# Optimization experiments

Measured on AMD Instinct MI355X. Metric: run time of the kernel, lower is better.

The kernel has to match this reference:

```python
import jax, jax.numpy as jnp
import numpy as np

N, E, H, L, G = 50000, 800000, 128, 4, 64

def setup_inputs() -> dict:
    key = jax.random.key(0)
    ks = jax.random.split(key, 16)
    s = 0.05
    x = jax.random.normal(ks[0], (N, H), jnp.float32)
    edge_index = jax.random.randint(ks[1], (2, E), 0, N)
    edge_attr = jax.random.normal(ks[2], (E, 1), jnp.float32)
    # sorted graph assignment covering all G graphs (batch[-1]+1 == G)
    batch = (jnp.arange(N) * G) // N
    conv_W1 = jax.random.normal(ks[3], (L, H, H), jnp.float32) * s
    conv_b1 = jnp.zeros((L, H), jnp.float32)
    conv_W2 = jax.random.normal(ks[4], (L, H, H), jnp.float32) * s
    conv_b2 = jnp.zeros((L, H), jnp.float32)
    conv_eps = jnp.zeros((L,), jnp.float32)  # torch init: eps = 0
    edge_W = jax.random.normal(ks[5], (L, 1, H), jnp.float32) * s
    edge_b = jnp.zeros((L, H), jnp.float32)
    vn_W1 = jax.random.normal(ks[6], (L - 1, H, H), jnp.float32) * s
    vn_b1 = jnp.zeros((L - 1, H), jnp.float32)
    vn_W2 = jax.random.normal(ks[7], (L - 1, H, H), jnp.float32) * s
    vn_b2 = jnp.zeros((L - 1, H), jnp.float32)
    vn_emb = jnp.zeros((H,), jnp.float32)  # torch init: constant 0
    return dict(x=x, edge_attr=edge_attr, conv_W1=conv_W1, conv_b1=conv_b1,
                conv_W2=conv_W2, conv_b2=conv_b2, conv_eps=conv_eps,
                edge_W=edge_W, edge_b=edge_b, vn_W1=vn_W1, vn_b1=vn_b1,
                vn_W2=vn_W2, vn_b2=vn_b2, vn_emb=vn_emb,
                edge_index=edge_index, batch=batch)


def reference(x, edge_attr, conv_W1, conv_b1, conv_W2, conv_b2, conv_eps,
              edge_W, edge_b, vn_W1, vn_b1, vn_W2, vn_b2, vn_emb,
              edge_index, batch):
    src, tgt = edge_index[0], edge_index[1]
    # PyG mean aggregation: divide scatter-sum by in-degree (clamped to 1)
    deg = jnp.maximum(
        jax.ops.segment_sum(jnp.ones((E,), x.dtype), tgt, num_segments=N), 1.0)[:, None]
    vn = jnp.broadcast_to(vn_emb[None, :], (G, H))  # virtual node per graph
    h = x
    hs = []
    for i in range(L):
        h = h + vn[batch]
        edge_emb = edge_attr @ edge_W[i] + edge_b[i]          # [E,H]
        msg = jax.nn.relu(h[src] + edge_emb)                   # gather + relu
        agg = jax.ops.segment_sum(msg, tgt, num_segments=N) / deg  # mean scatter
        z = (1.0 + conv_eps[i]) * h + agg
        h = jax.nn.relu(z @ conv_W1[i] + conv_b1[i]) @ conv_W2[i] + conv_b2[i]
        hs.append(h)
        if i < L - 1:
            vt = jax.ops.segment_sum(hs[i], batch, num_segments=G) + vn
            vn = jax.nn.relu(
                jax.nn.relu(vt @ vn_W1[i] + vn_b1[i]) @ vn_W2[i] + vn_b2[i])
            # eval mode: dropout is identity
    return jnp.concatenate(hs, axis=1)  # [N, L*H] jumping-knowledge concat
```

## Files before the change

kernel.cpp:

```cpp
#include <hip/hip_runtime.h>

#define NN 50000
#define EE 800000
#define HH 128
#define LL 4
#define GG 64
#define NR 50048
#define NS 8
#define CAP 64

typedef short bf16x8 __attribute__((ext_vector_type(8)));
typedef float f32x4 __attribute__((ext_vector_type(4)));

__device__ __forceinline__ unsigned bf_round(float f) {
  unsigned u = __float_as_uint(f);
  return (u + 0x7fffu + ((u >> 16) & 1u)) >> 16;
}
__device__ __forceinline__ unsigned bf_pack2(float lo, float hi) {
  return bf_round(lo) | (bf_round(hi) << 16);
}

__global__ __launch_bounds__(256) void init_pack0_kernel(
    int initB,
    const float* __restrict__ W1, const float* __restrict__ W2,
    const float* __restrict__ emb, short* __restrict__ wt1, short* __restrict__ wt2,
    float* __restrict__ vnA, float* __restrict__ part01, int* __restrict__ cur,
    const float4* __restrict__ x4, const float* __restrict__ eb0,
    uint2* __restrict__ hbf, int N) {
  int bid = blockIdx.x;
  int t = threadIdx.x;
  const int NW = 2 * LL * HH * HH;
  const int R1 = NW + GG * HH;
  const int R2 = R1 + 2 * GG * HH;
  const int R3 = R2 + NN;
  if (bid < initB) {
    int idx = bid * 256 + t;
    if (idx < NW) {
      int m = idx >> 14;
      int r = idx & 16383;
      int n = r >> 7, k = r & 127;
      const float* W = (m < LL) ? (W1 + (size_t)m * 16384) : (W2 + (size_t)(m - LL) * 16384);
      short* D = (m < LL) ? (wt1 + (size_t)m * 16384) : (wt2 + (size_t)(m - LL) * 16384);
      D[n * 128 + k] = (short)bf_round(W[k * 128 + n]);
    } else if (idx < R1) {
      int i = idx - NW;
      vnA[i] = emb[i & (HH - 1)];
    } else if (idx < R2) {
      part01[idx - R1] = 0.f;
    } else if (idx < R3) {
      cur[idx - R2] = 0;
    }
    return;
  }
  int pidx = (bid - initB) * 256 + t;
  if (pidx >= N * (HH / 4)) return;
  int c4 = pidx & 31;
  float4 a = x4[pidx];
  const float4 v = *(const float4*)(emb + c4 * 4);
  const float4 e = *(const float4*)(eb0 + c4 * 4);
  uint2 o;
  o.x = bf_pack2(a.x + v.x + e.x, a.y + v.y + e.y);
  o.y = bf_pack2(a.z + v.z + e.z, a.w + v.w + e.w);
  hbf[pidx] = o;
}

__global__ __launch_bounds__(256) void scatter_kernel(const int* __restrict__ src,
                                                      const int* __restrict__ tgt,
                                                      const float* __restrict__ attr,
                                                      int* __restrict__ cur,
                                                      int2* __restrict__ es, int E) {
  int e = blockIdx.x * 256 + threadIdx.x;
  if (e < E) {
    int t = tgt[e];
    int p = atomicAdd(&cur[t], 1);
    int2 rec;
    rec.x = src[e];
    rec.y = __float_as_int(attr[e]);
    es[(size_t)t * CAP + p] = rec;
  }
}

__device__ __forceinline__ void accum8s(float* acc, uint4 p, float a, float m,
                                        const float4& ew0, const float4& ew1) {
  acc[0] = fmaf(m, fmaxf(fmaf(a, ew0.x, __uint_as_float(p.x << 16)), 0.f), acc[0]);
  acc[1] = fmaf(m, fmaxf(fmaf(a, ew0.y, __uint_as_float(p.x & 0xffff0000u)), 0.f), acc[1]);
  acc[2] = fmaf(m, fmaxf(fmaf(a, ew0.z, __uint_as_float(p.y << 16)), 0.f), acc[2]);
  acc[3] = fmaf(m, fmaxf(fmaf(a, ew0.w, __uint_as_float(p.y & 0xffff0000u)), 0.f), acc[3]);
  acc[4] = fmaf(m, fmaxf(fmaf(a, ew1.x, __uint_as_float(p.z << 16)), 0.f), acc[4]);
  acc[5] = fmaf(m, fmaxf(fmaf(a, ew1.y, __uint_as_float(p.z & 0xffff0000u)), 0.f), acc[5]);
  acc[6] = fmaf(m, fmaxf(fmaf(a, ew1.z, __uint_as_float(p.w << 16)), 0.f), acc[6]);
  acc[7] = fmaf(m, fmaxf(fmaf(a, ew1.w, __uint_as_float(p.w & 0xffff0000u)), 0.f), acc[7]);
}

__global__ __launch_bounds__(128) void agg_kernel(const uint4* __restrict__ hbf4,
                                                  const float* __restrict__ hp, int pitch,
                                                  const float* __restrict__ vnp,
                                                  const int* __restrict__ batch,
                                                  const int2* __restrict__ es,
                                                  const int* __restrict__ cnp,
                                                  const float* __restrict__ eW,
                                                  const float* __restrict__ epsp,
                                                  uint4* __restrict__ zb4, int N) {
  int wave = threadIdx.x >> 6;
  int lane = threadIdx.x & 63;
  int n = blockIdx.x * 2 + wave;
  if (n >= N) return;
  int q = lane >> 4;
  int c = lane & 15;
  float4 ew0 = *(const float4*)(eW + c * 8);
  float4 ew1 = *(const float4*)(eW + c * 8 + 4);
  int cnt = cnp[n];
  const int2* eb = es + (size_t)n * CAP;
  float acc[8];
#pragma unroll
  for (int j = 0; j < 8; ++j) acc[j] = 0.f;
  for (int k = 0; k < cnt; k += 16) {
    int2 e0 = eb[min(k + q, cnt - 1)];
    int2 e1 = eb[min(k + 4 + q, cnt - 1)];
    int2 e2 = eb[min(k + 8 + q, cnt - 1)];
    int2 e3 = eb[min(k + 12 + q, cnt - 1)];
    uint4 p0 = hbf4[(size_t)e0.x * 16 + c];
    uint4 p1 = hbf4[(size_t)e1.x * 16 + c];
    uint4 p2 = hbf4[(size_t)e2.x * 16 + c];
    uint4 p3 = hbf4[(size_t)e3.x * 16 + c];
    float m0 = (k + q < cnt) ? 1.f : 0.f;
    float m1 = (k + 4 + q < cnt) ? 1.f : 0.f;
    float m2 = (k + 8 + q < cnt) ? 1.f : 0.f;
    float m3 = (k + 12 + q < cnt) ? 1.f : 0.f;
    accum8s(acc, p0, __int_as_float(e0.y), m0, ew0, ew1);
    accum8s(acc, p1, __int_as_float(e1.y), m1, ew0, ew1);
    accum8s(acc, p2, __int_as_float(e2.y), m2, ew0, ew1);
    accum8s(acc, p3, __int_as_float(e3.y), m3, ew0, ew1);
  }
#pragma unroll
  for (int j = 0; j < 8; ++j) {
    acc[j] += __shfl_xor(acc[j], 16);
    acc[j] += __shfl_xor(acc[j], 32);
  }
  int g = batch[n];
  const float* hrow = hp + (size_t)n * pitch + c * 8;
  const float* vrow = vnp + g * HH + c * 8;
  float4 h0 = *(const float4*)(hrow);
  float4 h1 = *(const float4*)(hrow + 4);
  float4 v0 = *(const float4*)(vrow);
  float4 v1 = *(const float4*)(vrow + 4);
  float inv = 1.f / fmaxf((float)cnt, 1.f);
  float onep = 1.f + epsp[0];
  uint4 o;
  o.x = bf_pack2(fmaf(onep, h0.x + v0.x, acc[0] * inv),
                 fmaf(onep, h0.y + v0.y, acc[1] * inv));
  o.y = bf_pack2(fmaf(onep, h0.z + v0.z, acc[2] * inv),
                 fmaf(onep, h0.w + v0.w, acc[3] * inv));
  o.z = bf_pack2(fmaf(onep, h1.x + v1.x, acc[4] * inv),
                 fmaf(onep, h1.y + v1.y, acc[5] * inv));
  o.w = bf_pack2(fmaf(onep, h1.z + v1.z, acc[6] * inv),
                 fmaf(onep, h1.w + v1.w, acc[7] * inv));
  if (q == 0) zb4[(size_t)n * 16 + c] = o;
}

__global__ __launch_bounds__(256) void mlp_kernel(const unsigned* __restrict__ zb,
                                                  const short* __restrict__ wt1,
                                                  const float* __restrict__ b1,
                                                  const short* __restrict__ wt2,
                                                  const float* __restrict__ b2,
                                                  float* __restrict__ out,
                                                  float* __restrict__ part,
                                                  int do_gs, int layer, int N) {
  __shared__ char smem[2 * 16 * 272];
  char* zr = smem;
  char* rr = smem + 16 * 272;
  int tid = threadIdx.x;
  int w = tid >> 6, lane = tid & 63;
  int l15 = lane & 15, q = lane >> 4;
  int row0 = blockIdx.x * 16;

  {
    int r = w * 4 + q;
    int c16 = l15;
    uint4 v = ((const uint4*)zb)[(size_t)(row0 + r) * 16 + c16];
    *(uint4*)(&zr[r * 272 + c16 * 16]) = v;
  }
  __syncthreads();

  f32x4 zero = {0.f, 0.f, 0.f, 0.f};
  f32x4 acc[2];
  acc[0] = zero; acc[1] = zero;

#pragma unroll
  for (int s = 0; s < 4; ++s) {
    bf16x8 af = *(const bf16x8*)(&zr[l15 * 272 + (s * 32 + q * 8) * 2]);
#pragma unroll
    for (int jj = 0; jj < 2; ++jj) {
      int j = w * 2 + jj;
      bf16x8 bf = *(const bf16x8*)(wt1 + (size_t)(j * 16 + l15) * 128 + s * 32 + q * 8);
      acc[jj] = __builtin_amdgcn_mfma_f32_16x16x32_bf16(af, bf, acc[jj], 0, 0, 0);
    }
  }
#pragma unroll
  for (int jj = 0; jj < 2; ++jj) {
    int j = w * 2 + jj;
    float bv = b1[j * 16 + l15];
#pragma unroll
    for (int r = 0; r < 4; ++r) {
      float v = fmaxf(acc[jj][r] + bv, 0.f);
      *(short*)(&rr[(q * 4 + r) * 272 + (j * 16 + l15) * 2]) = (short)bf_round(v);
    }
    acc[jj] = zero;
  }
  __syncthreads();
#pragma unroll
  for (int s = 0; s < 4; ++s) {
    bf16x8 af = *(const bf16x8*)(&rr[l15 * 272 + (s * 32 + q * 8) * 2]);
#pragma unroll
    for (int jj = 0; jj < 2; ++jj) {
      int j = w * 2 + jj;
      bf16x8 bf = *(const bf16x8*)(wt2 + (size_t)(j * 16 + l15) * 128 + s * 32 + q * 8);
      acc[jj] = __builtin_amdgcn_mfma_f32_16x16x32_bf16(af, bf, acc[jj], 0, 0, 0);
    }
  }
  int g0 = (int)(((long long)row0 * GG) / NN);
#pragma unroll
  for (int jj = 0; jj < 2; ++jj) {
    int j = w * 2 + jj;
    float bv = b2[j * 16 + l15];
    float s0 = 0.f, s1 = 0.f;
#pragma unroll
    for (int r = 0; r < 4; ++r) {
      int row = row0 + q * 4 + r;
      if (row < N) {
        float v = acc[jj][r] + bv;
        out[(size_t)row * (LL * HH) + layer * HH + j * 16 + l15] = v;
        if (do_gs) {
          int rel = (int)(((long long)row * GG) / NN) - g0;
          if (rel == 0) s0 += v; else s1 += v;
        }
      }
    }
    if (do_gs) {
      s0 += __shfl_xor(s0, 16); s0 += __shfl_xor(s0, 32);
      s1 += __shfl_xor(s1, 16); s1 += __shfl_xor(s1, 32);
      if (q == 0) {
        atomicAdd(&part[g0 * HH + j * 16 + l15], s0);
        if (s1 != 0.f) atomicAdd(&part[(g0 + 1) * HH + j * 16 + l15], s1);
      }
    }
  }
}

__global__ __launch_bounds__(256) void vnpack_kernel(const float* __restrict__ part_in,
                                                     float* __restrict__ part_zero,
                                                     const float* __restrict__ vn_in,
                                                     float* __restrict__ vn_out,
                                                     const float* __restrict__ W1,
                                                     const float* __restrict__ b1,
                                                     const float* __restrict__ W2,
                                                     const float* __restrict__ b2,
                                                     const float* __restrict__ outp,
                                                     const float* __restrict__ ebn,
                                                     uint2* __restrict__ hbf,
                                                     int layer, int N) {
  int b = blockIdx.x;
  int g = b >> 3, s = b & (NS - 1);
  int t = threadIdx.x;
  __shared__ float vr[128];
  __shared__ float tr[128];
  __shared__ float vo[128];
  if (t < 128) vr[t] = vn_in[g * HH + t] + part_in[g * HH + t];
  __syncthreads();
  if (t < 128) {
    float a = b1[t];
    for (int k = 0; k < 128; ++k) a = fmaf(vr[k], W1[k * HH + t], a);
    tr[t] = fmaxf(a, 0.f);
  }
  __syncthreads();
  if (t < 128) {
    float o = b2[t];
    for (int k = 0; k < 128; ++k) o = fmaf(tr[k], W2[k * HH + t], o);
    float vn = fmaxf(o, 0.f);
    vo[t] = vn;
    if (s == 0) {
      vn_out[g * HH + t] = vn;
      part_zero[g * HH + t] = 0.f;
    }
  }
  __syncthreads();
  int r0 = (g * NN + GG - 1) / GG;
  int r1 = ((g + 1) * NN + GG - 1) / GG;
  if (r1 > N) r1 = N;
  int len = r1 - r0;
  int chunk = (len + NS - 1) / NS;
  int rs = r0 + s * chunk;
  int re = min(rs + chunk, r1);
  int c4 = t & 31;
  float4 v = *(const float4*)(vo + c4 * 4);
  float4 e = *(const float4*)(ebn + c4 * 4);
  const float4* o4 = (const float4*)outp;
  for (int n = rs + (t >> 5); n < re; n += 8) {
    float4 a = o4[(size_t)n * (LL * HH / 4) + layer * (HH / 4) + c4];
    uint2 o;
    o.x = bf_pack2(a.x + v.x + e.x, a.y + v.y + e.y);
    o.y = bf_pack2(a.z + v.z + e.z, a.w + v.w + e.w);
    hbf[(size_t)n * 32 + c4] = o;
  }
}

extern "C" void kernel_launch(void* const* d_in, const int* in_sizes, int n_in,
                              void* d_out, int out_size, void* d_ws, size_t ws_size,
                              hipStream_t stream) {
  const int N = NN, E = EE, H = HH, L = LL, G = GG;
  const float* x          = (const float*)d_in[0];
  const float* edge_attr  = (const float*)d_in[1];
  const float* conv_W1    = (const float*)d_in[2];
  const float* conv_b1    = (const float*)d_in[3];
  const float* conv_W2    = (const float*)d_in[4];
  const float* conv_b2    = (const float*)d_in[5];
  const float* conv_eps   = (const float*)d_in[6];
  const float* edge_W     = (const float*)d_in[7];
  const float* edge_b     = (const float*)d_in[8];
  const float* vn_W1      = (const float*)d_in[9];
  const float* vn_b1      = (const float*)d_in[10];
  const float* vn_W2      = (const float*)d_in[11];
  const float* vn_b2      = (const float*)d_in[12];
  const float* vn_emb     = (const float*)d_in[13];
  const int*   edge_index = (const int*)d_in[14];
  const int*   batch      = (const int*)d_in[15];
  float* out = (float*)d_out;

  const int nbE = (E + 255) / 256;

  char* ws = (char*)d_ws;
  size_t off = 0;
  auto take = [&](size_t bytes) -> void* {
    void* p = ws + off;
    off = (off + bytes + 255) & ~(size_t)255;
    return p;
  };
  int*      cur   = (int*)take((size_t)N * 4);
  int2*     es    = (int2*)take((size_t)N * CAP * 8);
  unsigned* hbf   = (unsigned*)take((size_t)N * (H / 2) * 4);
  unsigned* zb    = (unsigned*)take((size_t)NR * (H / 2) * 4);
  short*    wt1   = (short*)take((size_t)L * H * H * 2);
  short*    wt2   = (short*)take((size_t)L * H * H * 2);
  float*    part  = (float*)take((size_t)2 * G * H * 4);
  float*    vnA   = (float*)take((size_t)G * H * 4);
  float*    vnB   = (float*)take((size_t)G * H * 4);

  const int* src = edge_index;
  const int* tgt = edge_index + E;

  const int initB = (2 * L * H * H + 3 * G * H + N + 255) / 256;
  const int packB = (N * (H / 4) + 255) / 256;
  init_pack0_kernel<<<initB + packB, 256, 0, stream>>>(
      initB, conv_W1, conv_W2, vn_emb, wt1, wt2, vnA, part, cur,
      (const float4*)x, edge_b, (uint2*)hbf, N);
  scatter_kernel<<<nbE, 256, 0, stream>>>(src, tgt, edge_attr, cur, es, E);

  for (int i = 0; i < L; ++i) {
    const float* hp;
    int pitch;
    if (i == 0) { hp = x; pitch = H; }
    else        { hp = out + (size_t)(i - 1) * H; pitch = L * H; }
    float* vin  = (i & 1) ? vnB : vnA;
    float* vout = (i & 1) ? vnA : vnB;
    agg_kernel<<<(N + 1) / 2, 128, 0, stream>>>(
        (const uint4*)hbf, hp, pitch, vin, batch, es, cur,
        edge_W + (size_t)i * H, conv_eps + i, (uint4*)zb, N);
    mlp_kernel<<<NR / 16, 256, 0, stream>>>(
        zb, wt1 + (size_t)i * H * H, conv_b1 + (size_t)i * H,
        wt2 + (size_t)i * H * H, conv_b2 + (size_t)i * H, out,
        part + (size_t)(i & 1) * G * H,
        (i < L - 1) ? 1 : 0, i, N);
    if (i < L - 1) {
      vnpack_kernel<<<G * NS, 256, 0, stream>>>(
          part + (size_t)(i & 1) * G * H,
          part + (size_t)((i + 1) & 1) * G * H,
          vin, vout,
          vn_W1 + (size_t)i * H * H, vn_b1 + (size_t)i * H,
          vn_W2 + (size_t)i * H * H, vn_b2 + (size_t)i * H,
          out, edge_b + (size_t)(i + 1) * H, (uint2*)hbf, i, N);
    }
  }
}
```

Baseline: 536.5 us.

## Fuse edge scatter into init kernel and widen MLP tile to 32 rows

```diff
diff --git a/kernel.cpp b/kernel.cpp
--- a/kernel.cpp
+++ b/kernel.cpp
@@ -20,21 +20,37 @@
   return bf_round(lo) | (bf_round(hi) << 16);
 }
 
-__global__ __launch_bounds__(256) void init_pack0_kernel(
-    int initB,
+__global__ __launch_bounds__(256) void scatter_init_pack0_kernel(
+    int scatB, int initB,
+    const int* __restrict__ src, const int* __restrict__ tgt,
+    const float* __restrict__ attr, int* __restrict__ cur, int2* __restrict__ es, int E,
     const float* __restrict__ W1, const float* __restrict__ W2,
     const float* __restrict__ emb, short* __restrict__ wt1, short* __restrict__ wt2,
-    float* __restrict__ vnA, float* __restrict__ part01, int* __restrict__ cur,
+    float* __restrict__ vnA, float* __restrict__ part01,
     const float4* __restrict__ x4, const float* __restrict__ eb0,
     uint2* __restrict__ hbf, int N) {
   int bid = blockIdx.x;
   int t = threadIdx.x;
-  const int NW = 2 * LL * HH * HH;
-  const int R1 = NW + GG * HH;
-  const int R2 = R1 + 2 * GG * HH;
-  const int R3 = R2 + NN;
-  if (bid < initB) {
-    int idx = bid * 256 + t;
+  if (bid < scatB) {
+#pragma unroll
+    for (int u = 0; u < 4; ++u) {
+      int e = bid * 1024 + u * 256 + t;
+      if (e < E) {
+        int tg = tgt[e];
+        int p = atomicAdd(&cur[tg], 1);
+        int2 rec;
+        rec.x = src[e];
+        rec.y = __float_as_int(attr[e]);
+        es[(size_t)tg * CAP + p] = rec;
+      }
+    }
+    return;
+  }
+  if (bid < scatB + initB) {
+    int idx = (bid - scatB) * 256 + t;
+    const int NW = 2 * LL * HH * HH;
+    const int R1 = NW + GG * HH;
+    const int R2 = R1 + 2 * GG * HH;
     if (idx < NW) {
       int m = idx >> 14;
       int r = idx & 16383;
@@ -47,12 +63,10 @@
       vnA[i] = emb[i & (HH - 1)];
     } else if (idx < R2) {
       part01[idx - R1] = 0.f;
-    } else if (idx < R3) {
-      cur[idx - R2] = 0;
     }
     return;
   }
-  int pidx = (bid - initB) * 256 + t;
+  int pidx = (bid - scatB - initB) * 256 + t;
   if (pidx >= N * (HH / 4)) return;
   int c4 = pidx & 31;
   float4 a = x4[pidx];
@@ -62,22 +76,6 @@
   o.x = bf_pack2(a.x + v.x + e.x, a.y + v.y + e.y);
   o.y = bf_pack2(a.z + v.z + e.z, a.w + v.w + e.w);
   hbf[pidx] = o;
-}
-
-__global__ __launch_bounds__(256) void scatter_kernel(const int* __restrict__ src,
-                                                      const int* __restrict__ tgt,
-                                                      const float* __restrict__ attr,
-                                                      int* __restrict__ cur,
-                                                      int2* __restrict__ es, int E) {
-  int e = blockIdx.x * 256 + threadIdx.x;
-  if (e < E) {
-    int t = tgt[e];
-    int p = atomicAdd(&cur[t], 1);
-    int2 rec;
-    rec.x = src[e];
-    rec.y = __float_as_int(attr[e]);
-    es[(size_t)t * CAP + p] = rec;
-  }
 }
 
 __device__ __forceinline__ void accum8s(float* acc, uint4 p, float a, float m,
@@ -166,34 +164,27 @@
                                                   float* __restrict__ out,
                                                   float* __restrict__ part,
                                                   int do_gs, int layer, int N) {
-  __shared__ char smem[2 * 16 * 272];
-  char* zr = smem;
-  char* rr = smem + 16 * 272;
+  __shared__ char rr[32 * 272];
   int tid = threadIdx.x;
   int w = tid >> 6, lane = tid & 63;
   int l15 = lane & 15, q = lane >> 4;
-  int row0 = blockIdx.x * 16;
-
-  {
-    int r = w * 4 + q;
-    int c16 = l15;
-    uint4 v = ((const uint4*)zb)[(size_t)(row0 + r) * 16 + c16];
-    *(uint4*)(&zr[r * 272 + c16 * 16]) = v;
-  }
-  __syncthreads();
+  int row0 = blockIdx.x * 32;
 
   f32x4 zero = {0.f, 0.f, 0.f, 0.f};
-  f32x4 acc[2];
-  acc[0] = zero; acc[1] = zero;
-
+  f32x4 acc[2][2];
+  acc[0][0] = zero; acc[0][1] = zero; acc[1][0] = zero; acc[1][1] = zero;
+
+  const char* zbase = (const char*)zb;
 #pragma unroll
   for (int s = 0; s < 4; ++s) {
-    bf16x8 af = *(const bf16x8*)(&zr[l15 * 272 + (s * 32 + q * 8) * 2]);
+    bf16x8 af0 = *(const bf16x8*)(zbase + (size_t)(row0 + l15) * 256 + (s * 32 + q * 8) * 2);
+    bf16x8 af1 = *(const bf16x8*)(zbase + (size_t)(row0 + 16 + l15) * 256 + (s * 32 + q * 8) * 2);
 #pragma unroll
     for (int jj = 0; jj < 2; ++jj) {
       int j = w * 2 + jj;
       bf16x8 bf = *(const bf16x8*)(wt1 + (size_t)(j * 16 + l15) * 128 + s * 32 + q * 8);
-      acc[jj] = __builtin_amdgcn_mfma_f32_16x16x32_bf16(af, bf, acc[jj], 0, 0, 0);
+      acc[jj][0] = __builtin_amdgcn_mfma_f32_16x16x32_bf16(af0, bf, acc[jj][0], 0, 0, 0);
+      acc[jj][1] = __builtin_amdgcn_mfma_f32_16x16x32_bf16(af1, bf, acc[jj][1], 0, 0, 0);
     }
   }
 #pragma unroll
@@ -201,21 +192,26 @@
     int j = w * 2 + jj;
     float bv = b1[j * 16 + l15];
 #pragma unroll
-    for (int r = 0; r < 4; ++r) {
-      float v = fmaxf(acc[jj][r] + bv, 0.f);
-      *(short*)(&rr[(q * 4 + r) * 272 + (j * 16 + l15) * 2]) = (short)bf_round(v);
-    }
-    acc[jj] = zero;
+    for (int rt = 0; rt < 2; ++rt) {
+#pragma unroll
+      for (int r = 0; r < 4; ++r) {
+        float v = fmaxf(acc[jj][rt][r] + bv, 0.f);
+        *(short*)(&rr[(rt * 16 + q * 4 + r) * 272 + (j * 16 + l15) * 2]) = (short)bf_round(v);
+      }
+      acc[jj][rt] = zero;
+    }
   }
   __syncthreads();
 #pragma unroll
   for (int s = 0; s < 4; ++s) {
-    bf16x8 af = *(const bf16x8*)(&rr[l15 * 272 + (s * 32 + q * 8) * 2]);
+    bf16x8 af0 = *(const bf16x8*)(&rr[l15 * 272 + (s * 32 + q * 8) * 2]);
+    bf16x8 af1 = *(const bf16x8*)(&rr[(16 + l15) * 272 + (s * 32 + q * 8) * 2]);
 #pragma unroll
     for (int jj = 0; jj < 2; ++jj) {
       int j = w * 2 + jj;
       bf16x8 bf = *(const bf16x8*)(wt2 + (size_t)(j * 16 + l15) * 128 + s * 32 + q * 8);
-      acc[jj] = __builtin_amdgcn_mfma_f32_16x16x32_bf16(af, bf, acc[jj], 0, 0, 0);
+      acc[jj][0] = __builtin_amdgcn_mfma_f32_16x16x32_bf16(af0, bf, acc[jj][0], 0, 0, 0);
+      acc[jj][1] = __builtin_amdgcn_mfma_f32_16x16x32_bf16(af1, bf, acc[jj][1], 0, 0, 0);
     }
   }
   int g0 = (int)(((long long)row0 * GG) / NN);
@@ -225,14 +221,17 @@
     float bv = b2[j * 16 + l15];
     float s0 = 0.f, s1 = 0.f;
 #pragma unroll
-    for (int r = 0; r < 4; ++r) {
-      int row = row0 + q * 4 + r;
-      if (row < N) {
-        float v = acc[jj][r] + bv;
-        out[(size_t)row * (LL * HH) + layer * HH + j * 16 + l15] = v;
-        if (do_gs) {
-          int rel = (int)(((long long)row * GG) / NN) - g0;
-          if (rel == 0) s0 += v; else s1 += v;
+    for (int rt = 0; rt < 2; ++rt) {
+#pragma unroll
+      for (int r = 0; r < 4; ++r) {
+        int row = row0 + rt * 16 + q * 4 + r;
+        if (row < N) {
+          float v = acc[jj][rt][r] + bv;
+          out[(size_t)row * (LL * HH) + layer * HH + j * 16 + l15] = v;
+          if (do_gs) {
+            int rel = (int)(((long long)row * GG) / NN) - g0;
+            if (rel == 0) s0 += v; else s1 += v;
+          }
         }
       }
     }
@@ -326,8 +325,6 @@
   const int*   batch      = (const int*)d_in[15];
   float* out = (float*)d_out;
 
-  const int nbE = (E + 255) / 256;
-
   char* ws = (char*)d_ws;
   size_t off = 0;
   auto take = [&](size_t bytes) -> void* {
@@ -348,12 +345,14 @@
   const int* src = edge_index;
   const int* tgt = edge_index + E;
 
-  const int initB = (2 * L * H * H + 3 * G * H + N + 255) / 256;
+  hipMemsetAsync(cur, 0, (size_t)N * 4, stream);
+  const int scatB = (E + 1023) / 1024;
+  const int initB = (2 * L * H * H + 3 * G * H + 255) / 256;
   const int packB = (N * (H / 4) + 255) / 256;
-  init_pack0_kernel<<<initB + packB, 256, 0, stream>>>(
-      initB, conv_W1, conv_W2, vn_emb, wt1, wt2, vnA, part, cur,
+  scatter_init_pack0_kernel<<<scatB + initB + packB, 256, 0, stream>>>(
+      scatB, initB, src, tgt, edge_attr, cur, es, E,
+      conv_W1, conv_W2, vn_emb, wt1, wt2, vnA, part,
       (const float4*)x, edge_b, (uint2*)hbf, N);
-  scatter_kernel<<<nbE, 256, 0, stream>>>(src, tgt, edge_attr, cur, es, E);
 
   for (int i = 0; i < L; ++i) {
     const float* hp;
@@ -365,7 +364,7 @@
     agg_kernel<<<(N + 1) / 2, 128, 0, stream>>>(
         (const uint4*)hbf, hp, pitch, vin, batch, es, cur,
         edge_W + (size_t)i * H, conv_eps + i, (uint4*)zb, N);
-    mlp_kernel<<<NR / 16, 256, 0, stream>>>(
+    mlp_kernel<<<NR / 32, 256, 0, stream>>>(
         zb, wt1 + (size_t)i * H * H, conv_b1 + (size_t)i * H,
         wt2 + (size_t)i * H * H, conv_b2 + (size_t)i * H, out,
         part + (size_t)(i & 1) * G * H,
```

New measurement: 514.2 us. 4.2% less time.
